# Kernel optimization log

Hardware: AMD Instinct MI355X
Metric: run time of the kernel (lower is better)

The kernel has to match this reference:

```python
import jax, jax.numpy as jnp
import numpy as np

# Model dims (from dispatcher config)
V, H, L, I, KD = 32000, 1024, 3, 4096, 256
NH, NKV, HD = 16, 4, 64          # head_dim = H/NH = KD/NKV = 64
G = NH // NKV                     # heads per KV group = 4
B, S = 2, 1024
BLOCK, NSUB = 512, 5              # process_output: first 5 subblocks of 512 rows
TOPL = 3                          # 'deep' focus -> top-3 layers


def setup_inputs() -> dict:
    key = jax.random.key(0)
    ks = jax.random.split(key, 16)
    w = lambda k, shape: jax.random.normal(k, shape, jnp.float32) * 0.02
    return {
        "input_ids": jax.random.randint(ks[0], (B, S), 0, V),
        "emb": w(ks[1], (V, H)),              # embedding_layer
        "shortcut_emb": w(ks[2], (1000, H)),  # shortcut_embed
        "Wq": w(ks[3], (L, H, H)),            # per-layer q_proj blocks (single block0 each)
        "Wk": w(ks[4], (L, KD, H)),
        "Wv": w(ks[5], (L, KD, H)),
        "Wo": w(ks[6], (L, H, H)),
        "Wgate": w(ks[7], (L, I, H)),
        "Wup": w(ks[8], (L, I, H)),
        "Wdown": w(ks[9], (L, H, I)),
        "Wls": w(ks[10], (L, H)),             # layer_scorer
        "bls": jnp.zeros((L,), jnp.float32),
        "Wbs": w(ks[11], (1, H)),             # block_scorer
        "bbs": jnp.zeros((1,), jnp.float32),
        "Wout": w(ks[12], (4096, H)),         # output weight block (split into 512-row subblocks)
    }


def _forward(input_ids, emb, shortcut_emb, Wq, Wk, Wv, Wo,
             Wgate, Wup, Wdown, Wls, bls, Wbs, bbs, Wout):
    b, s = input_ids.shape
    # is_common: all ids < 1000 -> shortcut embedding (prev_context None on fresh call)
    is_common = jnp.all(input_ids < 1000)
    h = jnp.where(is_common,
                  shortcut_emb[jnp.clip(input_ids, 0, 999)],
                  emb[input_ids])                       # [B,S,H]

    # select_layers ('deep' focus): top-3 layers by layer_scorer on batch elem 0
    layer_scores = h.mean(axis=1)[0] @ Wls.T + bls      # [L]
    _, sel = jax.lax.top_k(layer_scores, TOPL)

    for i in range(TOPL):
        li = sel[i]                                     # dynamic layer gather
        wq, wk, wv, wo = Wq[li], Wk[li], Wv[li], Wo[li]
        wg, wu, wd = Wgate[li], Wup[li], Wdown[li]

        # scan_layer: quick q projection -> block_scorer sigmoid gate
        quick_q = h @ wq.T                              # [B,S,H]
        gate = jax.nn.sigmoid(quick_q.mean(axis=1) @ Wbs.T + bbs) > 0.5  # [B,1]

        # process_attention: manual GQA with threshold-masked softmax
        q = (h @ wq.T).reshape(b, s, NKV, G, HD).transpose(0, 2, 3, 1, 4)  # [B,KV,G,S,D]
        k = (h @ wk.T).reshape(b, s, NKV, HD).transpose(0, 2, 1, 3)        # [B,KV,S,D]
        v = (h @ wv.T).reshape(b, s, NKV, HD).transpose(0, 2, 1, 3)        # [B,KV,S,D]
        scores = jnp.einsum('bhgsd,bhqd->bhgsq', q, k) / (HD ** 0.5)       # [B,KV,G,S,S]
        aw = jax.nn.softmax(scores, axis=-1)
        aw = aw * (aw > 0.01)                           # hard threshold mask
        v_exp = jnp.broadcast_to(v[:, :, None], (b, NKV, G, s, HD))
        # NOTE: faithful to source einsum 'bhgsq,bhgsd->bhgsd': sums aw over q and scales v
        attn = jnp.einsum('bhgsq,bhgsd->bhgsd', aw, v_exp)
        attn = attn.transpose(0, 3, 1, 2, 4).reshape(b, s, H)
        attn = attn @ wo.T

        # process_mlp: gate*up (no activation in source), then down
        new_h = ((attn @ wg.T) * (attn @ wu.T)) @ wd.T

        h = jnp.where(gate[:, :, None], new_h, h)       # scan_layer gate per batch elem

    # process_output: concat first 5 subblocks of 512 rows, matmul with transpose
    combined = Wout[:BLOCK * NSUB]                      # [2560, H]
    return h @ combined.T                               # [B,S,2560]


def reference(input_ids, emb, shortcut_emb, Wq, Wk, Wv, Wo,
              Wgate, Wup, Wdown, Wls, bls, Wbs, bbs, Wout):
    return _forward(input_ids, emb, shortcut_emb, Wq, Wk, Wv, Wo,
                    Wgate, Wup, Wdown, Wls, bls, Wbs, bbs, Wout)
```

## Files before the change

kernel.cpp:

```cpp
#include <hip/hip_runtime.h>
#include <hip/hip_bf16.h>

constexpr int kH = 1024, kS = 1024, kNH = 16, kI = 4096, kNOUT = 2560;
constexpr int kQKVN = 1536;

typedef __attribute__((ext_vector_type(8))) short short8v;
typedef __attribute__((ext_vector_type(4))) float f32x4;
typedef unsigned short u16;

#define MFMA16 __builtin_amdgcn_mfma_f32_16x16x32_bf16

__device__ __forceinline__ u16 f2bf(float f) {
  unsigned u = __float_as_uint(f);
  return (u16)((u + 0x7fffu + ((u >> 16) & 1u)) >> 16);
}
__device__ __forceinline__ float bf2f(u16 u) {
  return __uint_as_float(((unsigned)u) << 16);
}
__device__ __forceinline__ unsigned cvt2bf(float lo, float hi) {
  unsigned r;
  asm("v_cvt_pk_bf16_f32 %0, %1, %2" : "=v"(r) : "v"(lo), "v"(hi));
  return r;
}
__device__ __forceinline__ void gload16(void* lds, const void* g) {
  __builtin_amdgcn_global_load_lds(
      (const __attribute__((address_space(1))) unsigned int*)g,
      (__attribute__((address_space(3))) unsigned int*)lds, 16, 0, 0);
}

constexpr long OFF_H    = 0;
constexpr long OFF_HMP  = OFF_H + 2097152;
constexpr long OFF_INT  = OFF_HMP + 16384;
constexpr long OFF_GV   = OFF_INT + 64;
constexpr long OFF_HBF  = OFF_GV + 3072;
constexpr long OFF_QKV  = OFF_HBF + 1048576;
constexpr long OFF_ATT  = OFF_QKV + 1572864;
constexpr long OFF_OBF  = OFF_ATT + 1048576;
constexpr long OFF_PBF  = OFF_OBF + 1048576;

__global__ void embed_gv_kernel(const int* __restrict__ ids, const float* __restrict__ emb,
                                const float* __restrict__ semb, const float* __restrict__ Wq,
                                const float* __restrict__ Wbs, float* __restrict__ h,
                                u16* __restrict__ hbf, float* __restrict__ gv) {
  int bid = blockIdx.x, tid = threadIdx.x;
  if (bid < 2048) {
    __shared__ int oks;
    if (tid == 0) oks = 1;
    __syncthreads();
    int ok = 1;
    for (int i = tid; i < 2048; i += 256) ok &= (ids[i] < 1000) ? 1 : 0;
    if (!ok) atomicAnd(&oks, 0);
    __syncthreads();
    int common = oks;
    long row = bid;
    int id = ids[row];
    int cid = id < 0 ? 0 : (id > 999 ? 999 : id);
    const float4* s4 = (const float4*)(common ? semb + (long)cid * kH : emb + (long)id * kH);
    float4 v = s4[tid];
    *((float4*)(h + row * kH) + tid) = v;
    ushort4 u;
    u.x = f2bf(v.x); u.y = f2bf(v.y); u.z = f2bf(v.z); u.w = f2bf(v.w);
    *((ushort4*)(hbf + row * kH) + tid) = u;
  } else {
    int q = bid - 2048;
    int l = q >> 6, j0 = (q & 63) * 16;
    int jj = tid & 15, cg = tid >> 4;
    const float* wq = Wq + (long)l * 1048576;
    float acc = 0.f;
    for (int c = cg * 64; c < cg * 64 + 64; ++c)
      acc += Wbs[c] * wq[(long)c * kH + j0 + jj];
    __shared__ float red[256];
    red[tid] = acc;
    __syncthreads();
    if (tid < 16) {
      float s = 0.f;
      #pragma unroll
      for (int g = 0; g < 16; ++g) s += red[g * 16 + tid];
      gv[l * 1024 + j0 + tid] = s;
    }
  }
}

template <int FIRST>
__global__ __launch_bounds__(256) void hmean_fused_kernel(
    const float* __restrict__ h, float* __restrict__ hmp, const float* __restrict__ gv,
    const float* __restrict__ Wls, const float* __restrict__ bls,
    const float* __restrict__ bbs, int* __restrict__ ip, int layer_i,
    int* __restrict__ cnt) {
  int tid = threadIdx.x;
  int c = blockIdx.x * 256 + tid, b = blockIdx.y, z = blockIdx.z;
  float a = 0.f;
  if (!ip[16 + b]) {
    const float* p = h + ((long)b << 20) + ((long)z << 17) + c;
    #pragma unroll 4
    for (int r = 0; r < 128; ++r) a += p[(long)r << 10];
  }
  hmp[z * 2048 + b * 1024 + c] = a;
  __threadfence();
  __syncthreads();
  __shared__ int lastf;
  if (tid == 0) lastf = (atomicAdd(cnt, 1) == 63) ? 1 : 0;
  __syncthreads();
  if (!lastf) return;
  __threadfence();

  float hm0[4], hm1[4];
  #pragma unroll
  for (int u = 0; u < 4; ++u) {
    int j = tid + u * 256;
    float s0 = 0.f, s1 = 0.f;
    #pragma unroll
    for (int z2 = 0; z2 < 8; ++z2) {
      s0 += hmp[z2 * 2048 + j];
      s1 += hmp[z2 * 2048 + 1024 + j];
    }
    hm0[u] = s0; hm1[u] = s1;
  }
  __shared__ float red[3][256];
  __shared__ int sli;
  int li;
  if constexpr (FIRST) {
    float a0 = 0.f, a1 = 0.f, a2 = 0.f;
    #pragma unroll
    for (int u = 0; u < 4; ++u) {
      int j = tid + u * 256;
      a0 += hm0[u] * Wls[j];
      a1 += hm0[u] * Wls[kH + j];
      a2 += hm0[u] * Wls[2 * kH + j];
    }
    red[0][tid] = a0; red[1][tid] = a1; red[2][tid] = a2;
    __syncthreads();
    for (int st = 128; st; st >>= 1) {
      if (tid < st) {
        red[0][tid] += red[0][tid + st];
        red[1][tid] += red[1][tid + st];
        red[2][tid] += red[2][tid + st];
      }
      __syncthreads();
    }
    if (tid == 0) {
      float sc[3] = {red[0][0] * (1.f / kS) + bls[0], red[1][0] * (1.f / kS) + bls[1],
                     red[2][0] * (1.f / kS) + bls[2]};
      int aa = 0;
      if (sc[1] > sc[aa]) aa = 1;
      if (sc[2] > sc[aa]) aa = 2;
      int b2 = -1; float bb = -3.4e38f;
      for (int i = 0; i < 3; ++i)
        if (i != aa && sc[i] > bb) { bb = sc[i]; b2 = i; }
      ip[1] = aa; ip[2] = b2; ip[3] = 3 - aa - b2;
      sli = aa;
    }
    __syncthreads();
    li = sli;
  } else {
    li = ip[1 + layer_i];
  }
  float g0 = 0.f, g1 = 0.f;
  #pragma unroll
  for (int u = 0; u < 4; ++u) {
    int j = tid + u * 256;
    float v = gv[li * 1024 + j];
    g0 += v * hm0[u];
    g1 += v * hm1[u];
  }
  __syncthreads();
  red[0][tid] = g0; red[1][tid] = g1;
  __syncthreads();
  for (int st = 128; st; st >>= 1) {
    if (tid < st) { red[0][tid] += red[0][tid + st]; red[1][tid] += red[1][tid + st]; }
    __syncthreads();
  }
  if (tid == 0) {
    int* g = ip + 4 + 2 * layer_i;
    g[0] = ((red[0][0] * (1.f / kS) + bbs[0]) > 0.f) ? 1 : 0;
    g[1] = ((red[1][0] * (1.f / kS) + bbs[0]) > 0.f) ? 1 : 0;
  }
}

template <int MODE>
__global__ __launch_bounds__(256) void gemm_bf_kernel(
    const u16* __restrict__ A, const float* __restrict__ Bf0, const float* __restrict__ Bf1,
    const float* __restrict__ Bf2, void* __restrict__ C0, void* __restrict__ C1,
    int N, int K, const int* __restrict__ li_p,
    const int* __restrict__ gate, const int* __restrict__ act,
    int* __restrict__ hzwr, const int* __restrict__ hz) {
  constexpr bool USE_B1 = (MODE == 2);
  __shared__ u16 As[128 * 64];
  __shared__ u16 Bs[64 * 64];
  __shared__ u16 Bs1[USE_B1 ? 64 * 64 : 8];

  const int m0 = blockIdx.y * 128, n0 = blockIdx.x * 64;
  const int tid = threadIdx.x;
  const int bb = m0 >> 10;

  if (MODE == 4 && hz != nullptr && hz[bb]) {
    int r = tid >> 1, cb = n0 + (tid & 1) * 32;
    float* c0 = (float*)C0 + (long)(m0 + r) * N + cb;
    float4 z4 = make_float4(0.f, 0.f, 0.f, 0.f);
    #pragma unroll
    for (int j = 0; j < 32; j += 4) *(float4*)(c0 + j) = z4;
    return;
  }
  if (gate != nullptr) {
    int g = gate[bb];
    int ac = (act != nullptr) ? act[bb] : 1;
    if (MODE == 3 && hzwr != nullptr && tid == 0 && blockIdx.x == 0 && (m0 & 1023) == 0) {
      if (g) hzwr[bb] = ac ? 0 : 1;
    }
    if (!g || !ac) return;
    if (MODE == 0 && hz != nullptr && hz[bb]) return;
  }

  long li = (MODE == 4) ? 0 : (long)(*li_p);
  const float* bsrc;
  const float* bsrc1 = nullptr;
  if constexpr (MODE == 0) {
    if (n0 < 1024)      bsrc = Bf0 + li * 1048576 + (long)n0 * kH;
    else if (n0 < 1280) bsrc = Bf1 + li * 262144 + (long)(n0 - 1024) * kH;
    else                bsrc = Bf2 + li * 262144 + (long)(n0 - 1280) * kH;
  } else if constexpr (MODE == 1) {
    bsrc = Bf0 + li * 1048576 + (long)n0 * kH;
  } else if constexpr (MODE == 2) {
    bsrc = Bf0 + li * 4194304 + (long)n0 * kH;
    bsrc1 = Bf1 + li * 4194304 + (long)n0 * kH;
  } else if constexpr (MODE == 3) {
    bsrc = Bf0 + li * 4194304 + (long)n0 * kI;
  } else {
    bsrc = Bf0 + (long)n0 * kH;
  }

  const int wave = tid >> 6, lane = tid & 63;
  const int lr = lane & 15, lg = lane >> 4;
  const int wm = wave >> 1, wn = wave & 1;

  f32x4 acc[4][2] = {};
  f32x4 acc1[USE_B1 ? 4 : 1][2] = {};

  const int sr = tid >> 3, sc8 = tid & 7;
  const int sr1 = (tid + 256) >> 3;

  for (int k0 = 0; k0 < K; k0 += 64) {
    #pragma unroll
    for (int j = 0; j < 4; ++j) {
      int c = tid + j * 256;
      int r = c >> 3, c8 = c & 7;
      gload16((char*)As + (wave * 64 + j * 256) * 16,
              A + (long)(m0 + r) * K + k0 + ((c8 ^ (r & 7)) * 8));
    }
    #pragma unroll
    for (int j = 0; j < 2; ++j) {
      int r = j ? sr1 : sr, c8 = sc8;
      const float* p = bsrc + (long)r * K + k0 + c8 * 8;
      float4 v0 = *(const float4*)p;
      float4 v1 = *(const float4*)(p + 4);
      union { short8v s8; unsigned u[4]; } uo;
      uo.u[0] = cvt2bf(v0.x, v0.y);
      uo.u[1] = cvt2bf(v0.z, v0.w);
      uo.u[2] = cvt2bf(v1.x, v1.y);
      uo.u[3] = cvt2bf(v1.z, v1.w);
      *(short8v*)((char*)Bs + ((r * 128 + c8 * 16) ^ ((r & 7) << 4))) = uo.s8;
      if constexpr (USE_B1) {
        const float* p1 = bsrc1 + (long)r * K + k0 + c8 * 8;
        float4 w0 = *(const float4*)p1;
        float4 w1 = *(const float4*)(p1 + 4);
        union { short8v s8; unsigned u[4]; } uo1;
        uo1.u[0] = cvt2bf(w0.x, w0.y);
        uo1.u[1] = cvt2bf(w0.z, w0.w);
        uo1.u[2] = cvt2bf(w1.x, w1.y);
        uo1.u[3] = cvt2bf(w1.z, w1.w);
        *(short8v*)((char*)Bs1 + ((r * 128 + c8 * 16) ^ ((r & 7) << 4))) = uo1.s8;
      }
    }
    __syncthreads();
    #pragma unroll
    for (int kh = 0; kh < 2; ++kh) {
      const int kb = kh * 64 + lg * 16;
      short8v av[4], bv[2], b1v[2];
      #pragma unroll
      for (int mi = 0; mi < 4; ++mi) {
        int r = wm * 64 + mi * 16 + lr;
        av[mi] = *(const short8v*)((const char*)As + ((r * 128 + kb) ^ ((r & 7) << 4)));
      }
      #pragma unroll
      for (int ni = 0; ni < 2; ++ni) {
        int r = wn * 32 + ni * 16 + lr;
        int byte = (r * 128 + kb) ^ ((r & 7) << 4);
        bv[ni] = *(const short8v*)((const char*)Bs + byte);
        if constexpr (USE_B1) b1v[ni] = *(const short8v*)((const char*)Bs1 + byte);
      }
      #pragma unroll
      for (int mi = 0; mi < 4; ++mi)
        #pragma unroll
        for (int ni = 0; ni < 2; ++ni) {
          acc[mi][ni] = MFMA16(av[mi], bv[ni], acc[mi][ni], 0, 0, 0);
          if constexpr (USE_B1)
            acc1[mi][ni] = MFMA16(av[mi], b1v[ni], acc1[mi][ni], 0, 0, 0);
        }
    }
    __syncthreads();
  }
  #pragma unroll
  for (int mi = 0; mi < 4; ++mi)
    #pragma unroll
    for (int ni = 0; ni < 2; ++ni)
      #pragma unroll
      for (int r = 0; r < 4; ++r) {
        long idx = (long)(m0 + wm * 64 + mi * 16 + lg * 4 + r) * N +
                   (n0 + wn * 32 + ni * 16 + lr);
        float v = acc[mi][ni][r];
        if constexpr (MODE == 0 || MODE == 1) ((u16*)C0)[idx] = f2bf(v);
        if constexpr (MODE == 2) ((u16*)C0)[idx] = f2bf(v * acc1[mi][ni][r]);
        if constexpr (MODE == 3) { ((float*)C0)[idx] = v; ((u16*)C1)[idx] = f2bf(v); }
        if constexpr (MODE == 4) ((float*)C0)[idx] = v;
      }
}

__global__ __launch_bounds__(256) void rowsum_kernel(
    const u16* __restrict__ QKV, const int* __restrict__ gate, int* __restrict__ act,
    const int* __restrict__ hz, u16* __restrict__ ATT) {
  int b = blockIdx.z;
  if (!gate[b] || hz[b]) return;
  int kvg = blockIdx.y, qt = blockIdx.x;
  int tid = threadIdx.x;
  int w = tid >> 6, lane = tid & 63, lr = lane & 15, lg = lane >> 4;

  __shared__ float sm[4][64], ss[4][64], st[4][64], srs[64];
  __shared__ int sflags;
  if (tid == 0) sflags = 0;

  long qrow = ((long)b << 10) + qt * 16 + lr;
  short8v qlo[4], qhi[4];
  #pragma unroll
  for (int hh = 0; hh < 4; ++hh) {
    const u16* qp = QKV + qrow * kQKVN + (kvg * 4 + hh) * 64 + lg * 8;
    qlo[hh] = *(const short8v*)qp;
    qhi[hh] = *(const short8v*)(qp + 32);
  }
  const u16* kb0 = QKV + (((long)b << 10) + w * 256 + lr) * kQKVN + 1024 + kvg * 64 + lg * 8;

  float s[4][4], pm[4][4];
  #pragma unroll
  for (int hh = 0; hh < 4; ++hh)
    #pragma unroll
    for (int i = 0; i < 4; ++i) { s[hh][i] = 0.f; pm[hh][i] = -3e38f; }
  for (int kt = 0; kt < 16; ++kt) {
    const u16* kp = kb0 + (long)kt * 16 * kQKVN;
    short8v klo = *(const short8v*)kp;
    short8v khi = *(const short8v*)(kp + 32);
    #pragma unroll
    for (int hh = 0; hh < 4; ++hh) {
      f32x4 c = {0.f, 0.f, 0.f, 0.f};
      c = MFMA16(qlo[hh], klo, c, 0, 0, 0);
      c = MFMA16(qhi[hh], khi, c, 0, 0, 0);
      #pragma unroll
      for (int i = 0; i < 4; ++i) {
        float x = c[i] * 0.125f;
        s[hh][i] += __expf(x);
        pm[hh][i] = fmaxf(pm[hh][i], x);
      }
    }
  }
  #pragma unroll
  for (int off = 1; off < 16; off <<= 1)
    #pragma unroll
    for (int hh = 0; hh < 4; ++hh)
      #pragma unroll
      for (int i = 0; i < 4; ++i) {
        s[hh][i] += __shfl_xor(s[hh][i], off);
        pm[hh][i] = fmaxf(pm[hh][i], __shfl_xor(pm[hh][i], off));
      }
  if (lr == 0)
    #pragma unroll
    for (int hh = 0; hh < 4; ++hh)
      #pragma unroll
      for (int i = 0; i < 4; ++i) {
        sm[w][hh * 16 + lg * 4 + i] = pm[hh][i];
        ss[w][hh * 16 + lg * 4 + i] = s[hh][i];
      }
  __syncthreads();
  float Mg[4][4], Sg[4][4];
  int myfl = 0;
  #pragma unroll
  for (int hh = 0; hh < 4; ++hh)
    #pragma unroll
    for (int i = 0; i < 4; ++i) {
      int q = hh * 16 + lg * 4 + i;
      float mm = fmaxf(fmaxf(sm[0][q], sm[1][q]), fmaxf(sm[2][q], sm[3][q]));
      float SS = ss[0][q] + ss[1][q] + ss[2][q] + ss[3][q];
      Mg[hh][i] = mm; Sg[hh][i] = SS;
      if (mm > 60.f) myfl |= 2;
      if (__expf(mm) > 0.01f * SS) myfl |= 1;
    }
  if (myfl) atomicOr(&sflags, myfl);
  __syncthreads();
  int flags = sflags;

  if (flags & 2) {
    #pragma unroll
    for (int hh = 0; hh < 4; ++hh)
      #pragma unroll
      for (int i = 0; i < 4; ++i) s[hh][i] = 0.f;
    for (int kt = 0; kt < 16; ++kt) {
      const u16* kp = kb0 + (long)kt * 16 * kQKVN;
      short8v klo = *(const short8v*)kp;
      short8v khi = *(const short8v*)(kp + 32);
      #pragma unroll
      for (int hh = 0; hh < 4; ++hh) {
        f32x4 c = {0.f, 0.f, 0.f, 0.f};
        c = MFMA16(qlo[hh], klo, c, 0, 0, 0);
        c = MFMA16(qhi[hh], khi, c, 0, 0, 0);
        #pragma unroll
        for (int i = 0; i < 4; ++i) s[hh][i] += __expf(c[i] * 0.125f - Mg[hh][i]);
      }
    }
    #pragma unroll
    for (int off = 1; off < 16; off <<= 1)
      #pragma unroll
      for (int hh = 0; hh < 4; ++hh)
        #pragma unroll
        for (int i = 0; i < 4; ++i) s[hh][i] += __shfl_xor(s[hh][i], off);
    if (lr == 0)
      #pragma unroll
      for (int hh = 0; hh < 4; ++hh)
        #pragma unroll
        for (int i = 0; i < 4; ++i) ss[w][hh * 16 + lg * 4 + i] = s[hh][i];
    __syncthreads();
    #pragma unroll
    for (int hh = 0; hh < 4; ++hh)
      #pragma unroll
      for (int i = 0; i < 4; ++i) {
        int q = hh * 16 + lg * 4 + i;
        Sg[hh][i] = ss[0][q] + ss[1][q] + ss[2][q] + ss[3][q];
      }
    __syncthreads();
  }
  float shift = (flags & 2) ? 1.f : 0.f;

  if (flags & 1) {
    float tt[4][4] = {};
    for (int kt = 0; kt < 16; ++kt) {
      const u16* kp = kb0 + (long)kt * 16 * kQKVN;
      short8v klo = *(const short8v*)kp;
      short8v khi = *(const short8v*)(kp + 32);
      #pragma unroll
      for (int hh = 0; hh < 4; ++hh) {
        f32x4 c = {0.f, 0.f, 0.f, 0.f};
        c = MFMA16(qlo[hh], klo, c, 0, 0, 0);
        c = MFMA16(qhi[hh], khi, c, 0, 0, 0);
        #pragma unroll
        for (int i = 0; i < 4; ++i) {
          float e = __expf(c[i] * 0.125f - shift * Mg[hh][i]);
          if (e > 0.01f * Sg[hh][i]) tt[hh][i] += e;
        }
      }
    }
    #pragma unroll
    for (int off = 1; off < 16; off <<= 1)
      #pragma unroll
      for (int hh = 0; hh < 4; ++hh)
        #pragma unroll
        for (int i = 0; i < 4; ++i) tt[hh][i] += __shfl_xor(tt[hh][i], off);
    if (lr == 0)
      #pragma unroll
      for (int hh = 0; hh < 4; ++hh)
        #pragma unroll
        for (int i = 0; i < 4; ++i) st[w][hh * 16 + lg * 4 + i] = tt[hh][i];
  }
  __syncthreads();
  if (tid < 64) {
    int hh = tid >> 4, q = tid & 15;
    int qq = hh * 16 + q;
    float T = (flags & 1) ? (st[0][qq] + st[1][qq] + st[2][qq] + st[3][qq]) : 0.f;
    float SS = ss[0][qq] + ss[1][qq] + ss[2][qq] + ss[3][qq];
    srs[qq] = T / SS;
    if (T > 0.f) atomicOr(act + b, 1);
  }
  __syncthreads();
  int hh = tid >> 6, rr = (tid >> 2) & 15, d0 = (tid & 3) * 16;
  float rv = srs[hh * 16 + rr];
  long row = ((long)b << 10) + qt * 16 + rr;
  const u16* vp = QKV + row * kQKVN + 1280 + kvg * 64 + d0;
  u16* op = ATT + row * kH + (kvg * 4 + hh) * 64 + d0;
  #pragma unroll
  for (int j = 0; j < 16; j += 4) {
    ushort4 v = *(const ushort4*)(vp + j);
    ushort4 o;
    o.x = f2bf(rv * bf2f(v.x)); o.y = f2bf(rv * bf2f(v.y));
    o.z = f2bf(rv * bf2f(v.z)); o.w = f2bf(rv * bf2f(v.w));
    *(ushort4*)(op + j) = o;
  }
}

extern "C" void kernel_launch(void* const* d_in, const int* in_sizes, int n_in,
                              void* d_out, int out_size, void* d_ws, size_t ws_size,
                              hipStream_t stream) {
  (void)in_sizes; (void)n_in; (void)out_size; (void)ws_size;
  const int*   ids  = (const int*)d_in[0];
  const float* emb  = (const float*)d_in[1];
  const float* semb = (const float*)d_in[2];
  const float* Wq   = (const float*)d_in[3];
  const float* Wk   = (const float*)d_in[4];
  const float* Wv   = (const float*)d_in[5];
  const float* Wo   = (const float*)d_in[6];
  const float* Wg   = (const float*)d_in[7];
  const float* Wu   = (const float*)d_in[8];
  const float* Wd   = (const float*)d_in[9];
  const float* Wls  = (const float*)d_in[10];
  const float* bls  = (const float*)d_in[11];
  const float* Wbs  = (const float*)d_in[12];
  const float* bbs  = (const float*)d_in[13];
  const float* Wout = (const float*)d_in[14];
  float* out = (float*)d_out;
  float* ws  = (float*)d_ws;

  float* h   = ws + OFF_H;
  float* hmp = ws + OFF_HMP;
  int* ip    = (int*)(ws + OFF_INT);
  int* sel   = ip + 1;
  int* gate  = ip + 4;
  int* act   = ip + 10;
  int* hzb   = ip + 16;
  int* cnt   = ip + 20;
  float* gv  = ws + OFF_GV;
  u16* hbf   = (u16*)(ws + OFF_HBF);
  u16* QKV   = (u16*)(ws + OFF_QKV);
  u16* ATT   = (u16*)(ws + OFF_ATT);
  u16* Obf   = (u16*)(ws + OFF_OBF);
  u16* Pbf   = (u16*)(ws + OFF_PBF);

  (void)hipMemsetAsync(ip, 0, 32 * sizeof(int), stream);
  embed_gv_kernel<<<2240, 256, 0, stream>>>(ids, emb, semb, Wq, Wbs, h, hbf, gv);

  for (int i = 0; i < 3; i++) {
    const int* li = sel + i;
    int* g_i = gate + 2 * i;
    int* a_i = act + 2 * i;

    if (i == 0)
      hmean_fused_kernel<1><<<dim3(4, 2, 8), 256, 0, stream>>>(h, hmp, gv, Wls, bls, bbs,
                                                               ip, 0, cnt + 0);
    else
      hmean_fused_kernel<0><<<dim3(4, 2, 8), 256, 0, stream>>>(h, hmp, gv, Wls, bls, bbs,
                                                               ip, i, cnt + i);
    gemm_bf_kernel<0><<<dim3(kQKVN / 64, 16), 256, 0, stream>>>(
        hbf, Wq, Wk, Wv, QKV, nullptr, kQKVN, kH, li, g_i, nullptr, nullptr, hzb);
    rowsum_kernel<<<dim3(64, 4, 2), 256, 0, stream>>>(QKV, g_i, a_i, hzb, ATT);
    gemm_bf_kernel<1><<<dim3(kH / 64, 16), 256, 0, stream>>>(
        ATT, Wo, nullptr, nullptr, Obf, nullptr, kH, kH, li, g_i, a_i, nullptr, nullptr);
    gemm_bf_kernel<2><<<dim3(kI / 64, 16), 256, 0, stream>>>(
        Obf, Wg, Wu, nullptr, Pbf, nullptr, kI, kH, li, g_i, a_i, nullptr, nullptr);
    gemm_bf_kernel<3><<<dim3(kH / 64, 16), 256, 0, stream>>>(
        Pbf, Wd, nullptr, nullptr, h, hbf, kH, kI, li, g_i, a_i, hzb, nullptr);
  }
  gemm_bf_kernel<4><<<dim3(kNOUT / 64, 16), 256, 0, stream>>>(
      hbf, Wout, nullptr, nullptr, out, nullptr, kNOUT, kH, nullptr, nullptr, nullptr,
      nullptr, hzb);
}
```

Baseline: 153.4 us.

## Fuse O-proj, gate/up and down GEMMs into one persistent kernel with grid barriers

Replaces the three per-layer MLP GEMM launches (Wo, gate*up, down) with a single persistent 256-block kernel that runs each phase in sequence, separated by atomic-counter device-wide barriers. It also folds the hipMemsetAsync of the control ints into an extra block of the embedding kernel. The aim is to cut kernel launch overhead and inter-kernel gaps. The risks are deadlock if the 256 blocks are not all co-resident, the cost of spin-wait barriers, and lower parallelism in the gate/up phase, where each block loops over 4 tiles.

```diff
diff --git a/kernel.cpp b/kernel.cpp
--- a/kernel.cpp
+++ b/kernel.cpp
@@ -41,7 +41,8 @@
 __global__ void embed_gv_kernel(const int* __restrict__ ids, const float* __restrict__ emb,
                                 const float* __restrict__ semb, const float* __restrict__ Wq,
                                 const float* __restrict__ Wbs, float* __restrict__ h,
-                                u16* __restrict__ hbf, float* __restrict__ gv) {
+                                u16* __restrict__ hbf, float* __restrict__ gv,
+                                int* __restrict__ ip) {
   int bid = blockIdx.x, tid = threadIdx.x;
   if (bid < 2048) {
     __shared__ int oks;
@@ -61,7 +62,7 @@
     ushort4 u;
     u.x = f2bf(v.x); u.y = f2bf(v.y); u.z = f2bf(v.z); u.w = f2bf(v.w);
     *((ushort4*)(hbf + row * kH) + tid) = u;
-  } else {
+  } else if (bid < 2240) {
     int q = bid - 2048;
     int l = q >> 6, j0 = (q & 63) * 16;
     int jj = tid & 15, cg = tid >> 4;
@@ -78,6 +79,8 @@
       for (int g = 0; g < 16; ++g) s += red[g * 16 + tid];
       gv[l * 1024 + j0 + tid] = s;
     }
+  } else {
+    if (tid < 32) ip[tid] = 0;
   }
 }
 
@@ -180,14 +183,11 @@
 template <int MODE>
 __global__ __launch_bounds__(256) void gemm_bf_kernel(
     const u16* __restrict__ A, const float* __restrict__ Bf0, const float* __restrict__ Bf1,
-    const float* __restrict__ Bf2, void* __restrict__ C0, void* __restrict__ C1,
+    const float* __restrict__ Bf2, void* __restrict__ C0,
     int N, int K, const int* __restrict__ li_p,
-    const int* __restrict__ gate, const int* __restrict__ act,
-    int* __restrict__ hzwr, const int* __restrict__ hz) {
-  constexpr bool USE_B1 = (MODE == 2);
+    const int* __restrict__ gate, const int* __restrict__ hz) {
   __shared__ u16 As[128 * 64];
   __shared__ u16 Bs[64 * 64];
-  __shared__ u16 Bs1[USE_B1 ? 64 * 64 : 8];
 
   const int m0 = blockIdx.y * 128, n0 = blockIdx.x * 64;
   const int tid = threadIdx.x;
@@ -201,32 +201,122 @@
     for (int j = 0; j < 32; j += 4) *(float4*)(c0 + j) = z4;
     return;
   }
-  if (gate != nullptr) {
-    int g = gate[bb];
-    int ac = (act != nullptr) ? act[bb] : 1;
-    if (MODE == 3 && hzwr != nullptr && tid == 0 && blockIdx.x == 0 && (m0 & 1023) == 0) {
-      if (g) hzwr[bb] = ac ? 0 : 1;
-    }
-    if (!g || !ac) return;
-    if (MODE == 0 && hz != nullptr && hz[bb]) return;
+  if (MODE == 0) {
+    if (!gate[bb]) return;
+    if (hz != nullptr && hz[bb]) return;
   }
 
   long li = (MODE == 4) ? 0 : (long)(*li_p);
   const float* bsrc;
-  const float* bsrc1 = nullptr;
   if constexpr (MODE == 0) {
     if (n0 < 1024)      bsrc = Bf0 + li * 1048576 + (long)n0 * kH;
     else if (n0 < 1280) bsrc = Bf1 + li * 262144 + (long)(n0 - 1024) * kH;
     else                bsrc = Bf2 + li * 262144 + (long)(n0 - 1280) * kH;
-  } else if constexpr (MODE == 1) {
-    bsrc = Bf0 + li * 1048576 + (long)n0 * kH;
-  } else if constexpr (MODE == 2) {
-    bsrc = Bf0 + li * 4194304 + (long)n0 * kH;
-    bsrc1 = Bf1 + li * 4194304 + (long)n0 * kH;
-  } else if constexpr (MODE == 3) {
-    bsrc = Bf0 + li * 4194304 + (long)n0 * kI;
   } else {
     bsrc = Bf0 + (long)n0 * kH;
+  }
+
+  const int wave = tid >> 6, lane = tid & 63;
+  const int lr = lane & 15, lg = lane >> 4;
+  const int wm = wave >> 1, wn = wave & 1;
+
+  f32x4 acc[4][2] = {};
+
+  const int sr = tid >> 3, sc8 = tid & 7;
+  const int sr1 = (tid + 256) >> 3;
+
+  for (int k0 = 0; k0 < K; k0 += 64) {
+    #pragma unroll
+    for (int j = 0; j < 4; ++j) {
+      int c = tid + j * 256;
+      int r = c >> 3, c8 = c & 7;
+      gload16((char*)As + (wave * 64 + j * 256) * 16,
+              A + (long)(m0 + r) * K + k0 + ((c8 ^ (r & 7)) * 8));
+    }
+    #pragma unroll
+    for (int j = 0; j < 2; ++j) {
+      int r = j ? sr1 : sr, c8 = sc8;
+      const float* p = bsrc + (long)r * K + k0 + c8 * 8;
+      float4 v0 = *(const float4*)p;
+      float4 v1 = *(const float4*)(p + 4);
+      union { short8v s8; unsigned u[4]; } uo;
+      uo.u[0] = cvt2bf(v0.x, v0.y);
+      uo.u[1] = cvt2bf(v0.z, v0.w);
+      uo.u[2] = cvt2bf(v1.x, v1.y);
+      uo.u[3] = cvt2bf(v1.z, v1.w);
+      *(short8v*)((char*)Bs + ((r * 128 + c8 * 16) ^ ((r & 7) << 4))) = uo.s8;
+    }
+    __syncthreads();
+    #pragma unroll
+    for (int kh = 0; kh < 2; ++kh) {
+      const int kb = kh * 64 + lg * 16;
+      short8v av[4], bv[2];
+      #pragma unroll
+      for (int mi = 0; mi < 4; ++mi) {
+        int r = wm * 64 + mi * 16 + lr;
+        av[mi] = *(const short8v*)((const char*)As + ((r * 128 + kb) ^ ((r & 7) << 4)));
+      }
+      #pragma unroll
+      for (int ni = 0; ni < 2; ++ni) {
+        int r = wn * 32 + ni * 16 + lr;
+        bv[ni] = *(const short8v*)((const char*)Bs + ((r * 128 + kb) ^ ((r & 7) << 4)));
+      }
+      #pragma unroll
+      for (int mi = 0; mi < 4; ++mi)
+        #pragma unroll
+        for (int ni = 0; ni < 2; ++ni)
+          acc[mi][ni] = MFMA16(av[mi], bv[ni], acc[mi][ni], 0, 0, 0);
+    }
+    __syncthreads();
+  }
+  #pragma unroll
+  for (int mi = 0; mi < 4; ++mi)
+    #pragma unroll
+    for (int ni = 0; ni < 2; ++ni)
+      #pragma unroll
+      for (int r = 0; r < 4; ++r) {
+        long idx = (long)(m0 + wm * 64 + mi * 16 + lg * 4 + r) * N +
+                   (n0 + wn * 32 + ni * 16 + lr);
+        float v = acc[mi][ni][r];
+        if constexpr (MODE == 0) ((u16*)C0)[idx] = f2bf(v);
+        else ((float*)C0)[idx] = v;
+      }
+}
+
+__device__ __forceinline__ void dev_barrier(int* cnt, int target) {
+  __syncthreads();
+  __threadfence();
+  if (threadIdx.x == 0) {
+    atomicAdd(cnt, 1);
+    while (atomicAdd(cnt, 0) < target) __builtin_amdgcn_s_sleep(8);
+  }
+  __syncthreads();
+  __threadfence();
+}
+
+template <int PH>
+__device__ __forceinline__ void mlp_tile(int t, long li, const u16* __restrict__ A,
+                                         const float* __restrict__ B0base,
+                                         const float* __restrict__ B1base,
+                                         void* __restrict__ C0, void* __restrict__ C1,
+                                         int ac0, int ac1, u16* As, u16* Bs, u16* Bs1) {
+  constexpr bool USE_B1 = (PH == 1);
+  constexpr int N = (PH == 1) ? 4096 : 1024;
+  constexpr int K = (PH == 2) ? 4096 : 1024;
+  const int tid = threadIdx.x;
+  const int tm = t & 15, tn = t >> 4;
+  const int m0 = tm * 128, n0 = tn * 64;
+  if (!((tm >> 3) ? ac1 : ac0)) return;
+
+  const float* bsrc;
+  const float* bsrc1 = nullptr;
+  if constexpr (PH == 0) {
+    bsrc = B0base + li * 1048576 + (long)n0 * 1024;
+  } else if constexpr (PH == 1) {
+    bsrc = B0base + li * 4194304 + (long)n0 * 1024;
+    bsrc1 = B1base + li * 4194304 + (long)n0 * 1024;
+  } else {
+    bsrc = B0base + li * 4194304 + (long)n0 * 4096;
   }
 
   const int wave = tid >> 6, lane = tid & 63;
@@ -308,11 +398,39 @@
         long idx = (long)(m0 + wm * 64 + mi * 16 + lg * 4 + r) * N +
                    (n0 + wn * 32 + ni * 16 + lr);
         float v = acc[mi][ni][r];
-        if constexpr (MODE == 0 || MODE == 1) ((u16*)C0)[idx] = f2bf(v);
-        if constexpr (MODE == 2) ((u16*)C0)[idx] = f2bf(v * acc1[mi][ni][r]);
-        if constexpr (MODE == 3) { ((float*)C0)[idx] = v; ((u16*)C1)[idx] = f2bf(v); }
-        if constexpr (MODE == 4) ((float*)C0)[idx] = v;
-      }
+        if constexpr (PH == 0) ((u16*)C0)[idx] = f2bf(v);
+        if constexpr (PH == 1) ((u16*)C0)[idx] = f2bf(v * acc1[mi][ni][r]);
+        if constexpr (PH == 2) { ((float*)C0)[idx] = v; ((u16*)C1)[idx] = f2bf(v); }
+      }
+}
+
+__global__ __launch_bounds__(256) void mlp_kernel(
+    const u16* __restrict__ ATT, const float* __restrict__ Wo, const float* __restrict__ Wg,
+    const float* __restrict__ Wu, const float* __restrict__ Wd, u16* __restrict__ Obf,
+    u16* __restrict__ Pbf, float* __restrict__ h, u16* __restrict__ hbf,
+    const int* __restrict__ li_p, const int* __restrict__ gate,
+    const int* __restrict__ act, int* __restrict__ hzwr, int* __restrict__ cnt2) {
+  const int tid = threadIdx.x, bid = blockIdx.x;
+  int g0 = gate[0], g1 = gate[1];
+  int a0 = act[0], a1 = act[1];
+  if (bid == 0 && tid == 0) {
+    if (g0) hzwr[0] = a0 ? 0 : 1;
+    if (g1) hzwr[1] = a1 ? 0 : 1;
+  }
+  int ac0 = g0 && a0, ac1 = g1 && a1;
+  if (!ac0 && !ac1) return;
+
+  __shared__ u16 As[128 * 64];
+  __shared__ u16 Bs[64 * 64];
+  __shared__ u16 Bs1[64 * 64];
+  long li = (long)(*li_p);
+
+  mlp_tile<0>(bid, li, ATT, Wo, nullptr, Obf, nullptr, ac0, ac1, As, Bs, Bs1);
+  dev_barrier(cnt2 + 0, 256);
+  for (int t = bid; t < 1024; t += 256)
+    mlp_tile<1>(t, li, Obf, Wg, Wu, Pbf, nullptr, ac0, ac1, As, Bs, Bs1);
+  dev_barrier(cnt2 + 1, 256);
+  mlp_tile<2>(bid, li, Pbf, Wd, nullptr, h, hbf, ac0, ac1, As, Bs, Bs1);
 }
 
 __global__ __launch_bounds__(256) void rowsum_kernel(
@@ -521,6 +639,7 @@
   int* act   = ip + 10;
   int* hzb   = ip + 16;
   int* cnt   = ip + 20;
+  int* bar   = ip + 24;
   float* gv  = ws + OFF_GV;
   u16* hbf   = (u16*)(ws + OFF_HBF);
   u16* QKV   = (u16*)(ws + OFF_QKV);
@@ -528,8 +647,7 @@
   u16* Obf   = (u16*)(ws + OFF_OBF);
   u16* Pbf   = (u16*)(ws + OFF_PBF);
 
-  (void)hipMemsetAsync(ip, 0, 32 * sizeof(int), stream);
-  embed_gv_kernel<<<2240, 256, 0, stream>>>(ids, emb, semb, Wq, Wbs, h, hbf, gv);
+  embed_gv_kernel<<<2241, 256, 0, stream>>>(ids, emb, semb, Wq, Wbs, h, hbf, gv, ip);
 
   for (int i = 0; i < 3; i++) {
     const int* li = sel + i;
@@ -543,16 +661,11 @@
       hmean_fused_kernel<0><<<dim3(4, 2, 8), 256, 0, stream>>>(h, hmp, gv, Wls, bls, bbs,
                                                                ip, i, cnt + i);
     gemm_bf_kernel<0><<<dim3(kQKVN / 64, 16), 256, 0, stream>>>(
-        hbf, Wq, Wk, Wv, QKV, nullptr, kQKVN, kH, li, g_i, nullptr, nullptr, hzb);
+        hbf, Wq, Wk, Wv, QKV, kQKVN, kH, li, g_i, hzb);
     rowsum_kernel<<<dim3(64, 4, 2), 256, 0, stream>>>(QKV, g_i, a_i, hzb, ATT);
-    gemm_bf_kernel<1><<<dim3(kH / 64, 16), 256, 0, stream>>>(
-        ATT, Wo, nullptr, nullptr, Obf, nullptr, kH, kH, li, g_i, a_i, nullptr, nullptr);
-    gemm_bf_kernel<2><<<dim3(kI / 64, 16), 256, 0, stream>>>(
-        Obf, Wg, Wu, nullptr, Pbf, nullptr, kI, kH, li, g_i, a_i, nullptr, nullptr);
-    gemm_bf_kernel<3><<<dim3(kH / 64, 16), 256, 0, stream>>>(
-        Pbf, Wd, nullptr, nullptr, h, hbf, kH, kI, li, g_i, a_i, hzb, nullptr);
+    mlp_kernel<<<256, 256, 0, stream>>>(ATT, Wo, Wg, Wu, Wd, Obf, Pbf, h, hbf,
+                                        li, g_i, a_i, hzb, bar + 2 * i);
   }
   gemm_bf_kernel<4><<<dim3(kNOUT / 64, 16), 256, 0, stream>>>(
-      hbf, Wout, nullptr, nullptr, out, nullptr, kNOUT, kH, nullptr, nullptr, nullptr,
-      nullptr, hzb);
-}
+      hbf, Wout, nullptr, nullptr, out, kNOUT, kH, nullptr, nullptr, hzb);
+}
```

Result: faster. 137.3 us (-10.5%).
